# Performance work log

Measured on AMD Instinct MI355X. Metric: run time of the kernel, lower is better.

Reference implementation:

```python
import jax, jax.numpy as jnp
import numpy as np

BN_EPS = 1e-5

def cbr(x, W, g, b, m, v):
    # 1x1 conv (no bias) + folded BatchNorm (inference) + ReLU.
    # x: [B, Cin, H, W], W: [Cout, Cin]
    y = jnp.einsum('bchw,oc->bohw', x, W)
    scale = g * jax.lax.rsqrt(v + BN_EPS)            # [Cout]
    shift = b - m * scale                            # [Cout]
    y = y * scale[None, :, None, None] + shift[None, :, None, None]
    return jax.nn.relu(y)

def setup_inputs() -> dict:
    key = jax.random.key(0)
    ks = iter(jax.random.split(key, 40))
    B, INC, KEYC, H, W, K = 8, 512, 256, 128, 128, 19
    d = {}
    d['x'] = jax.random.normal(next(ks), (B, INC, H, W), jnp.float32)
    d['proxy'] = jax.random.normal(next(ks), (B, INC, K, 1), jnp.float32)
    def wmat(o, i):
        return jax.random.normal(next(ks), (o, i), jnp.float32) * 0.05
    def bnp(c):
        return (jax.random.uniform(next(ks), (c,), jnp.float32),
                jax.random.normal(next(ks), (c,), jnp.float32),
                jax.random.normal(next(ks), (c,), jnp.float32),
                jax.random.uniform(next(ks), (c,), jnp.float32))
    d['pw1'] = wmat(KEYC, INC); d['pg1'], d['pb1'], d['pm1'], d['pv1'] = bnp(KEYC)
    d['pw2'] = wmat(KEYC, KEYC); d['pg2'], d['pb2'], d['pm2'], d['pv2'] = bnp(KEYC)
    d['ow1'] = wmat(KEYC, INC); d['og1'], d['ob1'], d['om1'], d['ov1'] = bnp(KEYC)
    d['ow2'] = wmat(KEYC, KEYC); d['og2'], d['ob2'], d['om2'], d['ov2'] = bnp(KEYC)
    d['dw'] = wmat(KEYC, INC); d['dg'], d['db'], d['dm'], d['dv'] = bnp(KEYC)
    d['uw'] = wmat(INC, KEYC); d['ug'], d['ub'], d['um'], d['uv'] = bnp(INC)
    return d

def reference(x, proxy,
              pw1, pg1, pb1, pm1, pv1, pw2, pg2, pb2, pm2, pv2,
              ow1, og1, ob1, om1, ov1, ow2, og2, ob2, om2, ov2,
              dw, dg, db, dm, dv,
              uw, ug, ub, um, uv):
    B, _, H, W = x.shape
    keyc = pw1.shape[0]
    # f_pixel: two conv1x1+BN+ReLU -> query [B, N, keyc]
    q = cbr(cbr(x, pw1, pg1, pb1, pm1, pv1), pw2, pg2, pb2, pm2, pv2)
    q = q.reshape(B, keyc, H * W).transpose(0, 2, 1)           # [B, N, keyc]
    # f_object -> key [B, keyc, K]
    k = cbr(cbr(proxy, ow1, og1, ob1, om1, ov1), ow2, og2, ob2, om2, ov2)
    k = k.reshape(B, keyc, -1)                                  # [B, keyc, K]
    # f_down -> value [B, K, keyc]
    v = cbr(proxy, dw, dg, db, dm, dv).reshape(B, keyc, -1).transpose(0, 2, 1)
    # scaled attention over K object proxies
    sim = jnp.einsum('bnc,bck->bnk', q, k) * (keyc ** -0.5)     # [B, N, K]
    attn = jax.nn.softmax(sim, axis=-1)
    ctx = jnp.einsum('bnk,bkc->bnc', attn, v)                   # [B, N, keyc]
    ctx = ctx.transpose(0, 2, 1).reshape(B, keyc, H, W)
    # f_up -> [B, inc, H, W]
    return cbr(ctx, uw, ug, ub, um, uv)
```

## Files before the change

### kernel.cpp

```cpp
#include <hip/hip_runtime.h>

typedef unsigned int u32;
typedef unsigned short u16;
typedef __attribute__((ext_vector_type(8))) short bf16x8;
typedef __attribute__((ext_vector_type(4))) float f32x4;

#define DEVI static __device__ __forceinline__

DEVI u16 f2bf(float f) {
    u32 u = __float_as_uint(f);
    u32 r = u + 0x7FFFu + ((u >> 16) & 1u);
    return (u16)(r >> 16);
}
DEVI float bf2f(u16 s) { return __uint_as_float(((u32)s) << 16); }
DEVI void split2(float a, u16& h, u16& l) {
    h = f2bf(a);
    l = f2bf(a - bf2f(h));
}
DEVI int swz(int row) { return (row & 3) ^ ((row >> 2) & 3); }

DEVI void gload16(const void* g, void* l) {
    __builtin_amdgcn_global_load_lds(
        (const __attribute__((address_space(1))) u32*)g,
        (__attribute__((address_space(3))) u32*)l, 16, 0, 0);
}

union U4 { uint4 v; u16 s[8]; };

__global__ __launch_bounds__(256) void pack_w1_kernel(const float* __restrict__ wsrc,
                                                      u16* __restrict__ ph, u16* __restrict__ pl) {
    int i = blockIdx.x * 256 + threadIdx.x;
    int s = i >> 10, rem = i & 1023;
    int rg = rem >> 6, l = rem & 63;
    int row = rg * 16 + (l >> 2);
    int col = s * 32 + (((l & 3) ^ ((l >> 2) & 3) ^ ((l >> 4) & 3)) * 8);
    U4 hh, ll;
#pragma unroll
    for (int e = 0; e < 8; ++e) split2(wsrc[(size_t)row * 512 + col + e], hh.s[e], ll.s[e]);
    *reinterpret_cast<uint4*>(&ph[(size_t)i * 8]) = hh.v;
    *reinterpret_cast<uint4*>(&pl[(size_t)i * 8]) = ll.v;
}
__global__ __launch_bounds__(256) void pack_w2_kernel(const float* __restrict__ wsrc,
                                                      u16* __restrict__ ph, u16* __restrict__ pl) {
    int i = blockIdx.x * 256 + threadIdx.x;
    int w_ = i >> 11, s2 = (i >> 8) & 7, ni = (i >> 6) & 3, l = i & 63;
    int row = w_ * 64 + ni * 16 + (l & 15);
    int col = s2 * 32 + (l >> 4) * 8;
    U4 hh, ll;
#pragma unroll
    for (int e = 0; e < 8; ++e) split2(wsrc[(size_t)row * 256 + col + e], hh.s[e], ll.s[e]);
    *reinterpret_cast<uint4*>(&ph[(size_t)i * 8]) = hh.v;
    *reinterpret_cast<uint4*>(&pl[(size_t)i * 8]) = ll.v;
}
__global__ __launch_bounds__(256) void pack_wu_kernel(const float* __restrict__ wsrc,
                                                      u16* __restrict__ ph, u16* __restrict__ pl) {
    int i = blockIdx.x * 256 + threadIdx.x;
    int o4 = i >> 12, wc = (i >> 11) & 1, s = (i >> 8) & 7, ni = (i >> 6) & 3, l = i & 63;
    int row = o4 * 128 + wc * 64 + ni * 16 + (l & 15);
    int col = s * 32 + (l >> 4) * 8;
    U4 hh, ll;
#pragma unroll
    for (int e = 0; e < 8; ++e) split2(wsrc[(size_t)row * 256 + col + e], hh.s[e], ll.s[e]);
    *reinterpret_cast<uint4*>(&ph[(size_t)i * 8]) = hh.v;
    *reinterpret_cast<uint4*>(&pl[(size_t)i * 8]) = ll.v;
}

struct KVArgs {
    const float *proxy;
    const float *ow1, *og1, *ob1, *om1, *ov1;
    const float *ow2, *og2, *ob2, *om2, *ov2;
    const float *dw,  *dg,  *db,  *dm,  *dv;
    float *kmat;
    float *vmat;
};
__global__ __launch_bounds__(256) void kv_kernel(KVArgs a) {
    __shared__ float pl[512 * 19];
    __shared__ float t1[256 * 19];
    const int t = threadIdx.x;
    const int b = blockIdx.x;
    const float* pb = a.proxy + (size_t)b * 512 * 19;
    for (int i = t; i < 512 * 19; i += 256) pl[i] = pb[i];
    __syncthreads();
    const int o = t;
    {
        float acc[19] = {0.f};
        const float* wr = a.ow1 + (size_t)o * 512;
        for (int c = 0; c < 512; ++c) {
            float wv = wr[c];
#pragma unroll
            for (int kk = 0; kk < 19; ++kk) acc[kk] += wv * pl[c * 19 + kk];
        }
        float sc = a.og1[o] * __frsqrt_rn(a.ov1[o] + 1e-5f);
        float sh = a.ob1[o] - a.om1[o] * sc;
#pragma unroll
        for (int kk = 0; kk < 19; ++kk) t1[o * 19 + kk] = fmaxf(acc[kk] * sc + sh, 0.f);
    }
    __syncthreads();
    {
        float acc[19] = {0.f};
        const float* wr = a.ow2 + (size_t)o * 256;
        for (int c = 0; c < 256; ++c) {
            float wv = wr[c];
#pragma unroll
            for (int kk = 0; kk < 19; ++kk) acc[kk] += wv * t1[c * 19 + kk];
        }
        float sc = a.og2[o] * __frsqrt_rn(a.ov2[o] + 1e-5f);
        float sh = a.ob2[o] - a.om2[o] * sc;
#pragma unroll
        for (int kk = 0; kk < 19; ++kk)
            a.kmat[((size_t)b * 256 + o) * 19 + kk] = fmaxf(acc[kk] * sc + sh, 0.f);
    }
    {
        float acc[19] = {0.f};
        const float* wr = a.dw + (size_t)o * 512;
        for (int c = 0; c < 512; ++c) {
            float wv = wr[c];
#pragma unroll
            for (int kk = 0; kk < 19; ++kk) acc[kk] += wv * pl[c * 19 + kk];
        }
        float sc = a.dg[o] * __frsqrt_rn(a.dv[o] + 1e-5f);
        float sh = a.db[o] - a.dm[o] * sc;
#pragma unroll
        for (int kk = 0; kk < 19; ++kk)
            a.vmat[((size_t)b * 19 + kk) * 256 + o] = fmaxf(acc[kk] * sc + sh, 0.f);
    }
}

struct AttnArgs { const float* q2f; const float* kmat; const float* vmat;
                  u16* ctxh; u16* ctxl; long long p_off; };
__global__ __launch_bounds__(256, 2) void attn_kernel(AttnArgs a) {
    __shared__ float qs[16 * 261];
    __shared__ float kl[4864];
    __shared__ float vl[4864];
    __shared__ float sp[4 * 16 * 19];
    const int t = threadIdx.x;
    const int px = t & 15, cg = t >> 4;
    const int w = t >> 6, l = t & 63;
    const size_t pl_ = (size_t)blockIdx.x * 16;
    const size_t gpx0 = (size_t)a.p_off + pl_;
    const int b = (int)(gpx0 >> 14);
    for (int i = t; i < 4864; i += 256) { kl[i] = a.kmat[(size_t)b * 4864 + i];
                                          vl[i] = a.vmat[(size_t)b * 4864 + i]; }
    {
        const float* src = a.q2f + pl_ * 256;
#pragma unroll
        for (int j = 0; j < 4; ++j) {
            int f = j * 256 + t;
            float4 v = reinterpret_cast<const float4*>(src)[f];
            int pr = f >> 6, col = (f & 63) * 4;
            *reinterpret_cast<float4*>(&qs[pr * 261 + col]) = v;
        }
    }
    __syncthreads();
    float sim[19];
#pragma unroll
    for (int kk = 0; kk < 19; ++kk) sim[kk] = 0.f;
#pragma unroll 4
    for (int i = 0; i < 16; ++i) {
        int c = cg * 16 + i;
        float qv = qs[px * 261 + c];
#pragma unroll
        for (int kk = 0; kk < 19; ++kk) sim[kk] += qv * kl[c * 19 + kk];
    }
#pragma unroll
    for (int kk = 0; kk < 19; ++kk) {
        sim[kk] += __shfl_xor(sim[kk], 16);
        sim[kk] += __shfl_xor(sim[kk], 32);
    }
    if ((l >> 4) == 0) {
#pragma unroll
        for (int kk = 0; kk < 19; ++kk) sp[w * 304 + px * 19 + kk] = sim[kk];
    }
    __syncthreads();
    float wgt[19];
    float mx = -1e30f;
#pragma unroll
    for (int kk = 0; kk < 19; ++kk) {
        float s0 = sp[px * 19 + kk] + sp[304 + px * 19 + kk]
                 + sp[608 + px * 19 + kk] + sp[912 + px * 19 + kk];
        wgt[kk] = s0 * 0.0625f;
        mx = fmaxf(mx, wgt[kk]);
    }
    float ssum = 0.f;
#pragma unroll
    for (int kk = 0; kk < 19; ++kk) { wgt[kk] = __expf(wgt[kk] - mx); ssum += wgt[kk]; }
    const float inv = 1.f / ssum;
#pragma unroll
    for (int kk = 0; kk < 19; ++kk) wgt[kk] *= inv;
    const int Pg = (int)gpx0 + px;
    const int tile = Pg >> 6;
    const int pgg = (Pg >> 4) & 3;
    u16* th = a.ctxh + (size_t)tile * 16384;
    u16* tl = a.ctxl + (size_t)tile * 16384;
#pragma unroll
    for (int jj = 0; jj < 2; ++jj) {
        const int j = cg * 2 + jj;
        const int s = j >> 2, l4c = j & 3;
        U4 hh, ll;
#pragma unroll
        for (int e = 0; e < 8; ++e) {
            int c = j * 8 + e;
            float acc = 0.f;
#pragma unroll
            for (int kk = 0; kk < 19; ++kk) acc += wgt[kk] * vl[kk * 256 + c];
            split2(acc, hh.s[e], ll.s[e]);
        }
        const int off = (s * 4 + pgg) * 512 + (l4c * 16 + px) * 8;
        *reinterpret_cast<uint4*>(&th[off]) = hh.v;
        *reinterpret_cast<uint4*>(&tl[off]) = ll.v;
    }
}

struct F12Args {
    const float* Xf;
    const u16 *W1h, *W1l, *W2h, *W2l;
    const float *g1, *b1, *m1, *v1;
    const float *g2, *b2, *m2, *v2;
    float* q2f;
    int m_off;
};
__global__ __launch_bounds__(256, 2) void fused12_kernel(F12Args a) {
    __shared__ char LB[81920];
    u16* xs = (u16*)LB;
    u16* wb = (u16*)(LB + 16384);
    u16* q1 = (u16*)LB;
    float* tf = (float*)LB;

    const int t = threadIdx.x;
    const int l = t & 63, w = t >> 6;
    const int wr = w >> 1, wc = w & 1;
    const int l15 = l & 15, l4 = l >> 4;
    const int mloc = blockIdx.x * 128;
    const int mg = a.m_off + mloc;
    const int bb = mg >> 14, nb = mg & 16383;

    f32x4 acc1[4][8];
#pragma unroll
    for (int mi = 0; mi < 4; ++mi)
#pragma unroll
        for (int ni = 0; ni < 8; ++ni) acc1[mi][ni] = f32x4{0.f, 0.f, 0.f, 0.f};

    float fxA[8], fxB[8];

    auto loadX = [&](int s) {
        const int px = t & 127, oa = t >> 7;
        const float* s0 = a.Xf + (((size_t)bb * 512 + s * 32 + oa * 8) << 14) + nb + px;
        const float* s1 = a.Xf + (((size_t)bb * 512 + s * 32 + (oa + 2) * 8) << 14) + nb + px;
#pragma unroll
        for (int e = 0; e < 8; ++e) { fxA[e] = s0[(size_t)e << 14]; fxB[e] = s1[(size_t)e << 14]; }
    };
    auto writeX = [&]() {
        const int px = t & 127, oa = t >> 7;
        U4 phA, plA, phB, plB;
#pragma unroll
        for (int e = 0; e < 8; ++e) { split2(fxA[e], phA.s[e], plA.s[e]);
                                      split2(fxB[e], phB.s[e], plB.s[e]); }
        int posA = px * 32 + ((oa ^ swz(px)) * 8);
        int posB = px * 32 + (((oa + 2) ^ swz(px)) * 8);
        *reinterpret_cast<uint4*>(&xs[posA]) = phA.v;
        *reinterpret_cast<uint4*>(&xs[4096 + posA]) = plA.v;
        *reinterpret_cast<uint4*>(&xs[posB]) = phB.v;
        *reinterpret_cast<uint4*>(&xs[4096 + posB]) = plB.v;
    };
    auto dmaW1 = [&](int s, int buf) {
        const u16* bh = a.W1h + (size_t)s * 8192 + l * 8;
        const u16* bl2 = a.W1l + (size_t)s * 8192 + l * 8;
#pragma unroll
        for (int g = 0; g < 4; ++g) {
            const int rg = w * 4 + g;
            gload16(bh + rg * 512, &wb[buf * 16384 + rg * 512]);
            gload16(bl2 + rg * 512, &wb[buf * 16384 + 8192 + rg * 512]);
        }
    };

    loadX(0); dmaW1(0, 0);
    writeX();
    __syncthreads();
    int cur = 0;
    for (int s = 0; s < 16; ++s) {
        if (s < 15) dmaW1(s + 1, cur ^ 1);
        bf16x8 ah[4], am[4];
#pragma unroll
        for (int mi = 0; mi < 4; ++mi) {
            int ar = wr * 64 + mi * 16 + l15;
            int ap = ar * 32 + ((l4 ^ swz(ar)) * 8);
            ah[mi] = *reinterpret_cast<const bf16x8*>(&xs[ap]);
            am[mi] = *reinterpret_cast<const bf16x8*>(&xs[4096 + ap]);
        }
#pragma unroll
        for (int ni = 0; ni < 8; ++ni) {
            int br = wc * 128 + ni * 16 + l15;
            int bp = cur * 16384 + br * 32 + ((l4 ^ swz(br)) * 8);
            bf16x8 bh = *reinterpret_cast<const bf16x8*>(&wb[bp]);
            bf16x8 bl_ = *reinterpret_cast<const bf16x8*>(&wb[8192 + bp]);
#pragma unroll
            for (int mi = 0; mi < 4; ++mi) {
                acc1[mi][ni] = __builtin_amdgcn_mfma_f32_16x16x32_bf16(ah[mi], bh, acc1[mi][ni], 0, 0, 0);
                acc1[mi][ni] = __builtin_amdgcn_mfma_f32_16x16x32_bf16(ah[mi], bl_, acc1[mi][ni], 0, 0, 0);
                acc1[mi][ni] = __builtin_amdgcn_mfma_f32_16x16x32_bf16(am[mi], bh, acc1[mi][ni], 0, 0, 0);
            }
        }
        __syncthreads();
        if (s < 15) {
            loadX(s + 1);
            writeX();
            __syncthreads();
        }
        cur ^= 1;
    }

    float scl1[8], shf1[8];
#pragma unroll
    for (int ni = 0; ni < 8; ++ni) {
        int o = wc * 128 + ni * 16 + l15;
        scl1[ni] = a.g1[o] * __frsqrt_rn(a.v1[o] + 1e-5f);
        shf1[ni] = a.b1[o] - a.m1[o] * scl1[ni];
    }
    float scl2[4], shf2[4];
#pragma unroll
    for (int ni = 0; ni < 4; ++ni) {
        int o = w * 64 + ni * 16 + l15;
        scl2[ni] = a.g2[o] * __frsqrt_rn(a.v2[o] + 1e-5f);
        shf2[ni] = a.b2[o] - a.m2[o] * scl2[ni];
    }

#pragma unroll
    for (int cp = 0; cp < 4; ++cp) {
        __syncthreads();
#pragma unroll
        for (int ni = 0; ni < 8; ++ni) {
            int o1 = wc * 128 + ni * 16 + l15;
#pragma unroll
            for (int r = 0; r < 4; ++r) {
                int row = wr * 16 + l4 * 4 + r;
                float y = fmaxf(acc1[cp][ni][r] * scl1[ni] + shf1[ni], 0.f);
                u16 h, lo; split2(y, h, lo);
                int pos = row * 280 + o1;
                q1[pos] = h;
                q1[8960 + pos] = lo;
            }
        }
        __syncthreads();

        f32x4 acc2[2][4];
#pragma unroll
        for (int m = 0; m < 2; ++m)
#pragma unroll
            for (int ni = 0; ni < 4; ++ni) acc2[m][ni] = f32x4{0.f, 0.f, 0.f, 0.f};

#pragma unroll
        for (int s2 = 0; s2 < 8; ++s2) {
            bf16x8 a2h[2], a2m[2];
#pragma unroll
            for (int m = 0; m < 2; ++m) {
                int ap = (m * 16 + l15) * 280 + (s2 * 4 + l4) * 8;
                a2h[m] = *reinterpret_cast<const bf16x8*>(&q1[ap]);
                a2m[m] = *reinterpret_cast<const bf16x8*>(&q1[8960 + ap]);
            }
            const size_t bo0 = (size_t)(w * 8 + s2) * 2048 + l * 8;
#pragma unroll
            for (int ni = 0; ni < 4; ++ni) {
                bf16x8 b2h = *reinterpret_cast<const bf16x8*>(&a.W2h[bo0 + ni * 512]);
                bf16x8 b2l = *reinterpret_cast<const bf16x8*>(&a.W2l[bo0 + ni * 512]);
#pragma unroll
                for (int m = 0; m < 2; ++m) {
                    acc2[m][ni] = __builtin_amdgcn_mfma_f32_16x16x32_bf16(a2h[m], b2h, acc2[m][ni], 0, 0, 0);
                    acc2[m][ni] = __builtin_amdgcn_mfma_f32_16x16x32_bf16(a2h[m], b2l, acc2[m][ni], 0, 0, 0);
                    acc2[m][ni] = __builtin_amdgcn_mfma_f32_16x16x32_bf16(a2m[m], b2h, acc2[m][ni], 0, 0, 0);
                }
            }
        }
        __syncthreads();

#pragma unroll
        for (int m = 0; m < 2; ++m)
#pragma unroll
            for (int ni = 0; ni < 4; ++ni) {
                int o2 = w * 64 + ni * 16 + l15;
#pragma unroll
                for (int r = 0; r < 4; ++r) {
                    int row = m * 16 + l4 * 4 + r;
                    tf[row * 260 + o2] = fmaxf(acc2[m][ni][r] * scl2[ni] + shf2[ni], 0.f);
                }
            }
        __syncthreads();
#pragma unroll
        for (int j = 0; j < 8; ++j) {
            int task = j * 256 + t;
            int row = task >> 6, c4 = task & 63;
            int gpx = mloc + (row >> 4) * 64 + cp * 16 + (row & 15);
            *reinterpret_cast<float4*>(&a.q2f[(size_t)gpx * 256 + c4 * 4]) =
                *reinterpret_cast<const float4*>(&tf[row * 260 + c4 * 4]);
        }
    }
}

struct GUArgs {
    const u16 *Ah, *Al, *Wh, *Wl;
    const float *gg, *bbv, *mmv, *vvv;
    float* Yf;
};
__global__ __launch_bounds__(256, 4) void gemm_up_kernel(GUArgs a) {
    __shared__ float ldsf[128 * 68];
    const int t = threadIdx.x;
    const int l = t & 63;
    const int w = t >> 6;
    const int wr = w >> 1, wc = w & 1;
    const int l15 = l & 15, l4 = l >> 4;
    const int id = blockIdx.y * 4 + blockIdx.x;
    const int wid = (id & 7) * 1024 + (id >> 3);
    const int o0 = (wid & 3) * 128;
    const int m  = (wid >> 2) * 64;
    const int bb = m >> 14;
    const int nb = m & 16383;

    f32x4 acc[2][4];
#pragma unroll
    for (int mi = 0; mi < 2; ++mi)
#pragma unroll
        for (int ni = 0; ni < 4; ++ni) acc[mi][ni] = f32x4{0.f, 0.f, 0.f, 0.f};

    const size_t aoff0 = (size_t)(wid >> 2) * 16384 + (size_t)(wr * 2) * 512 + l * 8;
    const size_t woff0 = (size_t)(((wid & 3) * 2 + wc) * 8) * 2048 + l * 8;

#pragma unroll 2
    for (int s = 0; s < 8; ++s) {
        const size_t as = aoff0 + (size_t)s * 2048;
        const size_t wso = woff0 + (size_t)s * 2048;
        bf16x8 ah[2], al[2], bh[4], bl[4];
#pragma unroll
        for (int mi = 0; mi < 2; ++mi) {
            ah[mi] = *reinterpret_cast<const bf16x8*>(a.Ah + as + mi * 512);
            al[mi] = *reinterpret_cast<const bf16x8*>(a.Al + as + mi * 512);
        }
#pragma unroll
        for (int ni = 0; ni < 4; ++ni) {
            bh[ni] = *reinterpret_cast<const bf16x8*>(a.Wh + wso + ni * 512);
            bl[ni] = *reinterpret_cast<const bf16x8*>(a.Wl + wso + ni * 512);
        }
#pragma unroll
        for (int mi = 0; mi < 2; ++mi)
#pragma unroll
            for (int ni = 0; ni < 4; ++ni) {
                acc[mi][ni] = __builtin_amdgcn_mfma_f32_16x16x32_bf16(ah[mi], bh[ni], acc[mi][ni], 0, 0, 0);
                acc[mi][ni] = __builtin_amdgcn_mfma_f32_16x16x32_bf16(ah[mi], bl[ni], acc[mi][ni], 0, 0, 0);
                acc[mi][ni] = __builtin_amdgcn_mfma_f32_16x16x32_bf16(al[mi], bh[ni], acc[mi][ni], 0, 0, 0);
            }
    }

    float scl[4], shf[4];
#pragma unroll
    for (int ni = 0; ni < 4; ++ni) {
        int o = o0 + wc * 64 + ni * 16 + l15;
        scl[ni] = a.gg[o] * __frsqrt_rn(a.vvv[o] + 1e-5f);
        shf[ni] = a.bbv[o] - a.mmv[o] * scl[ni];
    }

#pragma unroll
    for (int ni = 0; ni < 4; ++ni) {
        int o_l = wc * 64 + ni * 16 + l15;
#pragma unroll
        for (int mi = 0; mi < 2; ++mi)
#pragma unroll
            for (int r = 0; r < 4; ++r) {
                int n_l = wr * 32 + mi * 16 + l4 * 4 + r;
                float y = fmaxf(acc[mi][ni][r] * scl[ni] + shf[ni], 0.f);
                ldsf[o_l * 68 + n_l] = y;
            }
    }
    __syncthreads();
#pragma unroll
    for (int j = 0; j < 8; ++j) {
        int idx = j * 256 + t;
        int row = idx >> 4, c4 = (idx & 15) * 4;
        *reinterpret_cast<float4*>(&a.Yf[((size_t)bb << 23) + (size_t)(o0 + row) * 16384 + nb + c4]) =
            *reinterpret_cast<const float4*>(&ldsf[row * 68 + c4]);
    }
}

extern "C" void kernel_launch(void* const* d_in, const int* in_sizes, int n_in,
                              void* d_out, int out_size, void* d_ws, size_t ws_size,
                              hipStream_t stream) {
    const float* x     = (const float*)d_in[0];
    const float* proxy = (const float*)d_in[1];
    const float* pw1 = (const float*)d_in[2];
    const float* pg1 = (const float*)d_in[3];
    const float* pb1 = (const float*)d_in[4];
    const float* pm1 = (const float*)d_in[5];
    const float* pv1 = (const float*)d_in[6];
    const float* pw2 = (const float*)d_in[7];
    const float* pg2 = (const float*)d_in[8];
    const float* pb2 = (const float*)d_in[9];
    const float* pm2 = (const float*)d_in[10];
    const float* pv2 = (const float*)d_in[11];
    const float* ow1 = (const float*)d_in[12];
    const float* og1 = (const float*)d_in[13];
    const float* ob1 = (const float*)d_in[14];
    const float* om1 = (const float*)d_in[15];
    const float* ov1 = (const float*)d_in[16];
    const float* ow2 = (const float*)d_in[17];
    const float* og2 = (const float*)d_in[18];
    const float* ob2 = (const float*)d_in[19];
    const float* om2 = (const float*)d_in[20];
    const float* ov2 = (const float*)d_in[21];
    const float* dw  = (const float*)d_in[22];
    const float* dg  = (const float*)d_in[23];
    const float* db  = (const float*)d_in[24];
    const float* dm  = (const float*)d_in[25];
    const float* dv  = (const float*)d_in[26];
    const float* uw  = (const float*)d_in[27];
    const float* ug  = (const float*)d_in[28];
    const float* ub  = (const float*)d_in[29];
    const float* um  = (const float*)d_in[30];
    const float* uv  = (const float*)d_in[31];

    char* ws = (char*)d_ws;
    u16* w1ph = (u16*)(ws + 0);
    u16* w1pl = (u16*)(ws + 262144);
    u16* w2ph = (u16*)(ws + 524288);
    u16* w2pl = (u16*)(ws + 655360);
    u16* wuph = (u16*)(ws + 786432);
    u16* wupl = (u16*)(ws + 1048576);
    float* kmat = (float*)(ws + 1310720);
    float* vmat = (float*)(ws + 1466368);
    u16* ctxh = (u16*)(ws + 2097152);
    u16* ctxl = (u16*)(ws + 69206016);
    float* q2f = (float*)(ws + 136314880ull);

    pack_w1_kernel<<<64, 256, 0, stream>>>(pw1, w1ph, w1pl);
    pack_w2_kernel<<<32, 256, 0, stream>>>(pw2, w2ph, w2pl);
    pack_wu_kernel<<<64, 256, 0, stream>>>(uw,  wuph, wupl);

    KVArgs ka{proxy, ow1, og1, ob1, om1, ov1, ow2, og2, ob2, om2, ov2,
              dw, dg, db, dm, dv, kmat, vmat};
    kv_kernel<<<8, 256, 0, stream>>>(ka);

    F12Args fa{x, w1ph, w1pl, w2ph, w2pl,
               pg1, pb1, pm1, pv1, pg2, pb2, pm2, pv2, q2f, 0};
    fused12_kernel<<<1024, 256, 0, stream>>>(fa);

    AttnArgs aa{q2f, kmat, vmat, ctxh, ctxl, 0};
    attn_kernel<<<8192, 256, 0, stream>>>(aa);

    GUArgs ga{ctxh, ctxl, wuph, wupl, ug, ub, um, uv, (float*)d_out};
    gemm_up_kernel<<<dim3(4, 2048), 256, 0, stream>>>(ga);
}
```

Measured before the change: 609.4 us.

## Fuse attention softmax and context into the fused conv1/conv2 kernel epilogue

Removes the separate attention kernel and the fp32 query buffer in global memory. The fused conv kernel now loads K/V into LDS and, for each 16-pixel chunk, computes the second conv, similarity, softmax and context in place, writing the split bf16 context directly. This avoids writing and re-reading the 128 MB query tensor and saves a kernel launch. In exchange the conv2 stage runs in smaller 16-row chunks with more barriers, lower MFMA reuse, and higher LDS pressure.

```diff
diff --git a/kernel.cpp b/kernel.cpp
--- a/kernel.cpp
+++ b/kernel.cpp
@@ -126,97 +126,13 @@
     }
 }
 
-struct AttnArgs { const float* q2f; const float* kmat; const float* vmat;
-                  u16* ctxh; u16* ctxl; long long p_off; };
-__global__ __launch_bounds__(256, 2) void attn_kernel(AttnArgs a) {
-    __shared__ float qs[16 * 261];
-    __shared__ float kl[4864];
-    __shared__ float vl[4864];
-    __shared__ float sp[4 * 16 * 19];
-    const int t = threadIdx.x;
-    const int px = t & 15, cg = t >> 4;
-    const int w = t >> 6, l = t & 63;
-    const size_t pl_ = (size_t)blockIdx.x * 16;
-    const size_t gpx0 = (size_t)a.p_off + pl_;
-    const int b = (int)(gpx0 >> 14);
-    for (int i = t; i < 4864; i += 256) { kl[i] = a.kmat[(size_t)b * 4864 + i];
-                                          vl[i] = a.vmat[(size_t)b * 4864 + i]; }
-    {
-        const float* src = a.q2f + pl_ * 256;
-#pragma unroll
-        for (int j = 0; j < 4; ++j) {
-            int f = j * 256 + t;
-            float4 v = reinterpret_cast<const float4*>(src)[f];
-            int pr = f >> 6, col = (f & 63) * 4;
-            *reinterpret_cast<float4*>(&qs[pr * 261 + col]) = v;
-        }
-    }
-    __syncthreads();
-    float sim[19];
-#pragma unroll
-    for (int kk = 0; kk < 19; ++kk) sim[kk] = 0.f;
-#pragma unroll 4
-    for (int i = 0; i < 16; ++i) {
-        int c = cg * 16 + i;
-        float qv = qs[px * 261 + c];
-#pragma unroll
-        for (int kk = 0; kk < 19; ++kk) sim[kk] += qv * kl[c * 19 + kk];
-    }
-#pragma unroll
-    for (int kk = 0; kk < 19; ++kk) {
-        sim[kk] += __shfl_xor(sim[kk], 16);
-        sim[kk] += __shfl_xor(sim[kk], 32);
-    }
-    if ((l >> 4) == 0) {
-#pragma unroll
-        for (int kk = 0; kk < 19; ++kk) sp[w * 304 + px * 19 + kk] = sim[kk];
-    }
-    __syncthreads();
-    float wgt[19];
-    float mx = -1e30f;
-#pragma unroll
-    for (int kk = 0; kk < 19; ++kk) {
-        float s0 = sp[px * 19 + kk] + sp[304 + px * 19 + kk]
-                 + sp[608 + px * 19 + kk] + sp[912 + px * 19 + kk];
-        wgt[kk] = s0 * 0.0625f;
-        mx = fmaxf(mx, wgt[kk]);
-    }
-    float ssum = 0.f;
-#pragma unroll
-    for (int kk = 0; kk < 19; ++kk) { wgt[kk] = __expf(wgt[kk] - mx); ssum += wgt[kk]; }
-    const float inv = 1.f / ssum;
-#pragma unroll
-    for (int kk = 0; kk < 19; ++kk) wgt[kk] *= inv;
-    const int Pg = (int)gpx0 + px;
-    const int tile = Pg >> 6;
-    const int pgg = (Pg >> 4) & 3;
-    u16* th = a.ctxh + (size_t)tile * 16384;
-    u16* tl = a.ctxl + (size_t)tile * 16384;
-#pragma unroll
-    for (int jj = 0; jj < 2; ++jj) {
-        const int j = cg * 2 + jj;
-        const int s = j >> 2, l4c = j & 3;
-        U4 hh, ll;
-#pragma unroll
-        for (int e = 0; e < 8; ++e) {
-            int c = j * 8 + e;
-            float acc = 0.f;
-#pragma unroll
-            for (int kk = 0; kk < 19; ++kk) acc += wgt[kk] * vl[kk * 256 + c];
-            split2(acc, hh.s[e], ll.s[e]);
-        }
-        const int off = (s * 4 + pgg) * 512 + (l4c * 16 + px) * 8;
-        *reinterpret_cast<uint4*>(&th[off]) = hh.v;
-        *reinterpret_cast<uint4*>(&tl[off]) = ll.v;
-    }
-}
-
 struct F12Args {
     const float* Xf;
     const u16 *W1h, *W1l, *W2h, *W2l;
     const float *g1, *b1, *m1, *v1;
     const float *g2, *b2, *m2, *v2;
-    float* q2f;
+    const float *kmat, *vmat;
+    u16 *ctxh, *ctxl;
     int m_off;
 };
 __global__ __launch_bounds__(256, 2) void fused12_kernel(F12Args a) {
@@ -225,13 +141,15 @@
     u16* wb = (u16*)(LB + 16384);
     u16* q1 = (u16*)LB;
     float* tf = (float*)LB;
+    float* sp = (float*)(LB + 16640);
+    float* kl = (float*)(LB + 21504);
+    float* vl = (float*)(LB + 40960);
 
     const int t = threadIdx.x;
     const int l = t & 63, w = t >> 6;
     const int wr = w >> 1, wc = w & 1;
     const int l15 = l & 15, l4 = l >> 4;
-    const int mloc = blockIdx.x * 128;
-    const int mg = a.m_off + mloc;
+    const int mg = a.m_off + blockIdx.x * 128;
     const int bb = mg >> 14, nb = mg & 16383;
 
     f32x4 acc1[4][8];
@@ -309,6 +227,12 @@
         cur ^= 1;
     }
 
+    {
+        const float* kb = a.kmat + (size_t)bb * 4864;
+        const float* vb = a.vmat + (size_t)bb * 4864;
+        for (int i = t; i < 4864; i += 256) { kl[i] = kb[i]; vl[i] = vb[i]; }
+    }
+
     float scl1[8], shf1[8];
 #pragma unroll
     for (int ni = 0; ni < 8; ++ni) {
@@ -324,73 +248,119 @@
         shf2[ni] = a.b2[o] - a.m2[o] * scl2[ni];
     }
 
-#pragma unroll
-    for (int cp = 0; cp < 4; ++cp) {
+    const int px16 = t & 15, cg = t >> 4;
+
+#pragma unroll
+    for (int ch = 0; ch < 8; ++ch) {
+        const int mi = ch & 3;
         __syncthreads();
-#pragma unroll
-        for (int ni = 0; ni < 8; ++ni) {
-            int o1 = wc * 128 + ni * 16 + l15;
-#pragma unroll
-            for (int r = 0; r < 4; ++r) {
-                int row = wr * 16 + l4 * 4 + r;
-                float y = fmaxf(acc1[cp][ni][r] * scl1[ni] + shf1[ni], 0.f);
-                u16 h, lo; split2(y, h, lo);
-                int pos = row * 280 + o1;
-                q1[pos] = h;
-                q1[8960 + pos] = lo;
+        if (wr == (ch >> 2)) {
+#pragma unroll
+            for (int ni = 0; ni < 8; ++ni) {
+                int o1 = wc * 128 + ni * 16 + l15;
+                int base = (o1 >> 3) * 8 + (o1 & 7);
+#pragma unroll
+                for (int r = 0; r < 4; ++r) {
+                    int px_l = l4 * 4 + r;
+                    float y = fmaxf(acc1[mi][ni][r] * scl1[ni] + shf1[ni], 0.f);
+                    u16 h, lo; split2(y, h, lo);
+                    int pos = px_l * 280 + base;
+                    q1[pos] = h;
+                    q1[4480 + pos] = lo;
+                }
             }
         }
         __syncthreads();
 
-        f32x4 acc2[2][4];
-#pragma unroll
-        for (int m = 0; m < 2; ++m)
-#pragma unroll
-            for (int ni = 0; ni < 4; ++ni) acc2[m][ni] = f32x4{0.f, 0.f, 0.f, 0.f};
-
+        f32x4 acc2[4];
+#pragma unroll
+        for (int ni = 0; ni < 4; ++ni) acc2[ni] = f32x4{0.f, 0.f, 0.f, 0.f};
 #pragma unroll
         for (int s2 = 0; s2 < 8; ++s2) {
-            bf16x8 a2h[2], a2m[2];
-#pragma unroll
-            for (int m = 0; m < 2; ++m) {
-                int ap = (m * 16 + l15) * 280 + (s2 * 4 + l4) * 8;
-                a2h[m] = *reinterpret_cast<const bf16x8*>(&q1[ap]);
-                a2m[m] = *reinterpret_cast<const bf16x8*>(&q1[8960 + ap]);
-            }
+            int ap = l15 * 280 + (s2 * 4 + l4) * 8;
+            bf16x8 a2h = *reinterpret_cast<const bf16x8*>(&q1[ap]);
+            bf16x8 a2m = *reinterpret_cast<const bf16x8*>(&q1[4480 + ap]);
             const size_t bo0 = (size_t)(w * 8 + s2) * 2048 + l * 8;
 #pragma unroll
             for (int ni = 0; ni < 4; ++ni) {
                 bf16x8 b2h = *reinterpret_cast<const bf16x8*>(&a.W2h[bo0 + ni * 512]);
                 bf16x8 b2l = *reinterpret_cast<const bf16x8*>(&a.W2l[bo0 + ni * 512]);
-#pragma unroll
-                for (int m = 0; m < 2; ++m) {
-                    acc2[m][ni] = __builtin_amdgcn_mfma_f32_16x16x32_bf16(a2h[m], b2h, acc2[m][ni], 0, 0, 0);
-                    acc2[m][ni] = __builtin_amdgcn_mfma_f32_16x16x32_bf16(a2h[m], b2l, acc2[m][ni], 0, 0, 0);
-                    acc2[m][ni] = __builtin_amdgcn_mfma_f32_16x16x32_bf16(a2m[m], b2h, acc2[m][ni], 0, 0, 0);
-                }
+                acc2[ni] = __builtin_amdgcn_mfma_f32_16x16x32_bf16(a2h, b2h, acc2[ni], 0, 0, 0);
+                acc2[ni] = __builtin_amdgcn_mfma_f32_16x16x32_bf16(a2h, b2l, acc2[ni], 0, 0, 0);
+                acc2[ni] = __builtin_amdgcn_mfma_f32_16x16x32_bf16(a2m, b2h, acc2[ni], 0, 0, 0);
             }
         }
         __syncthreads();
 
 #pragma unroll
-        for (int m = 0; m < 2; ++m)
-#pragma unroll
-            for (int ni = 0; ni < 4; ++ni) {
-                int o2 = w * 64 + ni * 16 + l15;
-#pragma unroll
-                for (int r = 0; r < 4; ++r) {
-                    int row = m * 16 + l4 * 4 + r;
-                    tf[row * 260 + o2] = fmaxf(acc2[m][ni][r] * scl2[ni] + shf2[ni], 0.f);
-                }
-            }
+        for (int ni = 0; ni < 4; ++ni) {
+            int o2 = w * 64 + ni * 16 + l15;
+#pragma unroll
+            for (int r = 0; r < 4; ++r) {
+                int px_l = l4 * 4 + r;
+                tf[px_l * 260 + o2] = fmaxf(acc2[ni][r] * scl2[ni] + shf2[ni], 0.f);
+            }
+        }
         __syncthreads();
-#pragma unroll
-        for (int j = 0; j < 8; ++j) {
-            int task = j * 256 + t;
-            int row = task >> 6, c4 = task & 63;
-            int gpx = mloc + (row >> 4) * 64 + cp * 16 + (row & 15);
-            *reinterpret_cast<float4*>(&a.q2f[(size_t)gpx * 256 + c4 * 4]) =
-                *reinterpret_cast<const float4*>(&tf[row * 260 + c4 * 4]);
+
+        float sim[19];
+#pragma unroll
+        for (int kk = 0; kk < 19; ++kk) sim[kk] = 0.f;
+#pragma unroll 4
+        for (int i = 0; i < 16; ++i) {
+            int c = cg * 16 + i;
+            float qv = tf[px16 * 260 + c];
+#pragma unroll
+            for (int kk = 0; kk < 19; ++kk) sim[kk] += qv * kl[c * 19 + kk];
+        }
+#pragma unroll
+        for (int kk = 0; kk < 19; ++kk) {
+            sim[kk] += __shfl_xor(sim[kk], 16);
+            sim[kk] += __shfl_xor(sim[kk], 32);
+        }
+        if ((l >> 4) == 0) {
+#pragma unroll
+            for (int kk = 0; kk < 19; ++kk) sp[w * 304 + px16 * 19 + kk] = sim[kk];
+        }
+        __syncthreads();
+
+        float wgt[19];
+        float mx = -1e30f;
+#pragma unroll
+        for (int kk = 0; kk < 19; ++kk) {
+            float s0 = sp[px16 * 19 + kk] + sp[304 + px16 * 19 + kk]
+                     + sp[608 + px16 * 19 + kk] + sp[912 + px16 * 19 + kk];
+            wgt[kk] = s0 * 0.0625f;
+            mx = fmaxf(mx, wgt[kk]);
+        }
+        float ssum = 0.f;
+#pragma unroll
+        for (int kk = 0; kk < 19; ++kk) { wgt[kk] = __expf(wgt[kk] - mx); ssum += wgt[kk]; }
+        const float inv = 1.f / ssum;
+#pragma unroll
+        for (int kk = 0; kk < 19; ++kk) wgt[kk] *= inv;
+
+        const int Pg = mg + ch * 16 + px16;
+        const int tile = Pg >> 6;
+        const int pgg = (Pg >> 4) & 3;
+        u16* th = a.ctxh + (size_t)tile * 16384;
+        u16* tl = a.ctxl + (size_t)tile * 16384;
+#pragma unroll
+        for (int jj = 0; jj < 2; ++jj) {
+            const int j = cg * 2 + jj;
+            const int s = j >> 2, l4c = j & 3;
+            U4 hh, ll;
+#pragma unroll
+            for (int e = 0; e < 8; ++e) {
+                int c = j * 8 + e;
+                float acc = 0.f;
+#pragma unroll
+                for (int kk = 0; kk < 19; ++kk) acc += wgt[kk] * vl[kk * 256 + c];
+                split2(acc, hh.s[e], ll.s[e]);
+            }
+            const int off = (s * 4 + pgg) * 512 + (l4c * 16 + px16) * 8;
+            *reinterpret_cast<uint4*>(&th[off]) = hh.v;
+            *reinterpret_cast<uint4*>(&tl[off]) = ll.v;
         }
     }
 }
@@ -525,7 +495,6 @@
     float* vmat = (float*)(ws + 1466368);
     u16* ctxh = (u16*)(ws + 2097152);
     u16* ctxl = (u16*)(ws + 69206016);
-    float* q2f = (float*)(ws + 136314880ull);
 
     pack_w1_kernel<<<64, 256, 0, stream>>>(pw1, w1ph, w1pl);
     pack_w2_kernel<<<32, 256, 0, stream>>>(pw2, w2ph, w2pl);
@@ -536,11 +505,8 @@
     kv_kernel<<<8, 256, 0, stream>>>(ka);
 
     F12Args fa{x, w1ph, w1pl, w2ph, w2pl,
-               pg1, pb1, pm1, pv1, pg2, pb2, pm2, pv2, q2f, 0};
+               pg1, pb1, pm1, pv1, pg2, pb2, pm2, pv2, kmat, vmat, ctxh, ctxl, 0};
     fused12_kernel<<<1024, 256, 0, stream>>>(fa);
-
-    AttnArgs aa{q2f, kmat, vmat, ctxh, ctxl, 0};
-    attn_kernel<<<8192, 256, 0, stream>>>(aa);
 
     GUArgs ga{ctxh, ctxl, wuph, wupl, ug, ub, um, uv, (float*)d_out};
     gemm_up_kernel<<<dim3(4, 2048), 256, 0, stream>>>(ga);
```

After: 885.9 us. +45.4%, slower.
